# Optimization experiments

Measured on AMD Instinct MI355X. Metric: run time of the kernel, lower is better.

## Reference

```python
import jax, jax.numpy as jnp
import numpy as np

BS, EP = 32, 32
N_AGENTS, N_ATOM, EMBED = 8, 51, 32
STATE_DIM, HYP = 128, 64
V_MIN, V_MAX = -10.0, 10.0


def proj(support, probs, v_min, v_max, n_atom):
    # C51 categorical projection of (support, probs) onto the fixed atom grid
    # linspace(v_min, v_max, n_atom). support/probs: [..., M] -> [..., n_atom]
    support, probs = jnp.broadcast_arrays(support, probs)
    delta = (v_max - v_min) / (n_atom - 1)
    b = (jnp.clip(support, v_min, v_max) - v_min) / delta
    l = jnp.floor(b)
    u = jnp.ceil(b)
    eq = (u == l).astype(probs.dtype)  # support exactly on an atom -> all mass to l
    ml = probs * (u - b + eq)
    mu = probs * (b - l)
    shp = probs.shape
    n = int(np.prod(shp[:-1]))
    m = shp[-1]
    rows = jnp.arange(n)[:, None]
    out = jnp.zeros((n, n_atom), probs.dtype)
    out = out.at[rows, l.astype(jnp.int32).reshape(n, m)].add(ml.reshape(n, m))
    out = out.at[rows, u.astype(jnp.int32).reshape(n, m)].add(mu.reshape(n, m))
    return out.reshape(shp[:-1] + (n_atom,))


def bconv(p, q):
    # Full 1D convolution of per-row categorical pmfs (sum of two random vars).
    # p: [N, L], q: [N, M] -> [N, L+M-1], via grouped conv (one group per row).
    N, L = p.shape
    M = q.shape[-1]
    out = jax.lax.conv_general_dilated(
        p[None], jnp.flip(q, -1)[:, None, :],
        window_strides=(1,), padding=[(M - 1, M - 1)],
        feature_group_count=N, dimension_numbers=('NCW', 'OIW', 'NCW'))
    return out[0]


def mlp2(x, w1, b1, w2, b2):
    return jax.nn.relu(x @ w1.T + b1) @ w2.T + b2


def setup_inputs():
    key = jax.random.key(0)
    ks = jax.random.split(key, 20)
    def p(k, shape, s=0.05):
        return jax.random.normal(k, shape, dtype=jnp.float32) * s
    aq = jax.random.uniform(ks[0], (BS, EP, N_AGENTS, N_ATOM), dtype=jnp.float32)
    aq = aq / jnp.sum(aq, -1, keepdims=True)  # valid categorical distributions
    return {
        'agent_qs_distri': aq,
        'states': p(ks[1], (BS, EP, STATE_DIM), 1.0),
        'hw1_w1': p(ks[2], (HYP, STATE_DIM)), 'hw1_b1': p(ks[3], (HYP,)),
        'hw1_w2': p(ks[4], (EMBED * N_AGENTS, HYP)), 'hw1_b2': p(ks[5], (EMBED * N_AGENTS,)),
        'hb1_w': p(ks[6], (EMBED, STATE_DIM)), 'hb1_b': p(ks[7], (EMBED,)),
        'hwf_w1': p(ks[8], (HYP, STATE_DIM)), 'hwf_b1': p(ks[9], (HYP,)),
        'hwf_w2': p(ks[10], (EMBED, HYP)), 'hwf_b2': p(ks[11], (EMBED,)),
        'v_w1': p(ks[12], (EMBED, STATE_DIM)), 'v_b1': p(ks[13], (EMBED,)),
        'v_w2': p(ks[14], (1, EMBED)), 'v_b2': p(ks[15], (1,)),
    }


def reference(agent_qs_distri, states, hw1_w1, hw1_b1, hw1_w2, hw1_b2,
              hb1_w, hb1_b, hwf_w1, hwf_b1, hwf_w2, hwf_b2,
              v_w1, v_b1, v_w2, v_b2):
    bs, ep, n_agents, n_atom = agent_qs_distri.shape
    s = states.reshape(-1, STATE_DIM)
    atoms = jnp.linspace(V_MIN, V_MAX, n_atom).astype(jnp.float32)  # [A]

    w1 = jnp.abs(mlp2(s, hw1_w1, hw1_b1, hw1_w2, hw1_b2)).reshape(bs, ep, EMBED, n_agents)
    b1 = (s @ hb1_w.T + hb1_b).reshape(bs, ep, EMBED)

    # stage 1: scale each agent's support by w1[..., k, i], project back onto atoms
    sup1 = atoms * w1[..., None]                                       # [bs,ep,E,Na,A]
    aw = proj(sup1, agent_qs_distri[:, :, None], V_MIN, V_MAX, n_atom)  # [bs,ep,E,Na,A]
    awf = aw.reshape(-1, n_agents, n_atom)                              # [bs*ep*E,Na,A]
    q = awf[:, 0]
    for i in range(1, n_agents):
        q = bconv(q, awf[:, i])                                         # [.., Na*A-Na+1]
    L1 = n_agents * n_atom - n_agents + 1
    sup = jnp.linspace(n_agents * V_MIN, n_agents * V_MAX, L1).astype(jnp.float32)
    sup = jax.nn.elu(sup + b1[..., None])                               # [bs,ep,E,L1]
    x = proj(sup, q.reshape(bs, ep, EMBED, L1), V_MIN, V_MAX, n_atom)   # [bs,ep,E,A]

    # stage 2: hyper_w_final scaling, convolve across embed dim, add V(s)
    wf = jnp.abs(mlp2(s, hwf_w1, hwf_b1, hwf_w2, hwf_b2)).reshape(bs, ep, EMBED)
    xw = proj(atoms * wf[..., None], x, V_MIN, V_MAX, n_atom)           # [bs,ep,E,A]
    xwf = xw.reshape(-1, EMBED, n_atom)
    q = xwf[:, 0]
    for i in range(1, EMBED):
        q = bconv(q, xwf[:, i])                                         # [bs*ep, E*A-E+1]
    L2 = EMBED * n_atom - EMBED + 1
    v = mlp2(s, v_w1, v_b1, v_w2, v_b2).reshape(bs, ep, 1)
    sup2 = jnp.linspace(EMBED * V_MIN, EMBED * V_MAX, L2).astype(jnp.float32) + v
    return proj(sup2, q.reshape(bs, ep, L2), V_MIN, V_MAX, n_atom)      # [bs,ep,A]
```

## Files before the change

kernel.cpp:

```cpp
#include <hip/hip_runtime.h>
#include <hip/hip_bf16.h>
#include <math.h>

typedef unsigned short u16;

#define WAVE_SYNC() asm volatile("s_waitcnt lgkmcnt(0)" ::: "memory")

__device__ __forceinline__ float bf2f(u16 u) {
  union { unsigned int i; float f; } c;
  c.i = ((unsigned int)u) << 16;
  return c.f;
}
__device__ __forceinline__ float bflo(unsigned int u) {
  union { unsigned int i; float f; } c; c.i = u << 16; return c.f;
}
__device__ __forceinline__ float bfhi(unsigned int u) {
  union { unsigned int i; float f; } c; c.i = u & 0xffff0000u; return c.f;
}
__device__ __forceinline__ u16 f2bf(float f) {
  union { float f; unsigned int i; } c;
  c.f = f;
  unsigned int x = c.i;
  unsigned int r = (x + 0x7fffu + ((x >> 16) & 1u)) >> 16;
  return (u16)r;
}

__device__ __forceinline__ void proj_bounds(float wv, int& ML, int& MH) {
  float smin = (-10.0f + 0.4f * 0.0f)  * wv;
  float smax = (-10.0f + 0.4f * 50.0f) * wv;
  float bmin = (fminf(fmaxf(smin, -10.0f), 10.0f) + 10.0f) / 0.4f;
  float bmax = (fminf(fmaxf(smax, -10.0f), 10.0f) + 10.0f) / 0.4f;
  ML = (int)floorf(bmin);
  MH = (int)ceilf(bmax);
}

__device__ __forceinline__ void conv_pad2(const float* __restrict__ q,
                                          float* __restrict__ qn,
                                          const float* __restrict__ kvs,
                                          int ML, int W, int T,
                                          int LQ, int HQ, int Jmax,
                                          int tid, int nthr)
{
  const int Lout = LQ + ML;
  const int Hout = min(HQ + ML + T, Jmax);
  for (int J = Lout + tid; J <= Hout; J += nthr) {
    const float* qp = q + (J - ML);
    float acc = 0.f;
    for (int c = 0; c < W; c += 4) {
      float4 k4 = *(const float4*)(kvs + c);
      acc = fmaf(k4.x, qp[-c],     acc);
      acc = fmaf(k4.y, qp[-c - 1], acc);
      acc = fmaf(k4.z, qp[-c - 2], acc);
      acc = fmaf(k4.w, qp[-c - 3], acc);
    }
    qn[J] = acc;
  }
}

__device__ __forceinline__ void conv16(const float* __restrict__ q,
                                       float* __restrict__ qn,
                                       const float* __restrict__ kvs,
                                       int ML, int T,
                                       int LQ, int HQ, int Jmax,
                                       int tid, int nthr)
{
  const int Lout = LQ + ML;
  const int Hout = min(HQ + ML + T, Jmax);
  for (int J = Lout + tid; J <= Hout; J += nthr) {
    const float* qp = q + (J - ML);
    float a0 = 0.f, a1 = 0.f;
#pragma unroll
    for (int c = 0; c < 16; c += 4) {
      float4 k4 = *(const float4*)(kvs + c);
      a0 = fmaf(k4.x, qp[-c],     a0);
      a1 = fmaf(k4.y, qp[-c - 1], a1);
      a0 = fmaf(k4.z, qp[-c - 2], a0);
      a1 = fmaf(k4.w, qp[-c - 3], a1);
    }
    qn[J] = a0 + a1;
  }
}

__device__ __forceinline__ void conv8(const float* __restrict__ q,
                                      float* __restrict__ qn,
                                      const float* __restrict__ kvs,
                                      int ML, int T,
                                      int LQ, int HQ, int Jmax,
                                      int tid, int nthr)
{
  const int Lout = LQ + ML;
  const int Hout = min(HQ + ML + T, Jmax);
  for (int J = Lout + tid; J <= Hout; J += nthr) {
    const float* qp = q + (J - ML);
    float a0 = 0.f, a1 = 0.f;
#pragma unroll
    for (int c = 0; c < 8; c += 4) {
      float4 k4 = *(const float4*)(kvs + c);
      a0 = fmaf(k4.x, qp[-c],     a0);
      a1 = fmaf(k4.y, qp[-c - 1], a1);
      a0 = fmaf(k4.z, qp[-c - 2], a0);
      a1 = fmaf(k4.w, qp[-c - 3], a1);
    }
    qn[J] = a0 + a1;
  }
}

template<int TA, int TB>
__device__ __forceinline__ float gather_part(const float* __restrict__ pb,
                                             float wv, float j)
{
  float a0 = 0.f, a1 = 0.f, a2 = 0.f, a3 = 0.f;
  const float4* pb4 = (const float4*)pb;
  const float base = 25.0f - j;
#pragma unroll
  for (int t4 = TA; t4 < TB; ++t4) {
    float4 p4 = pb4[t4];
#define G1(PX, TT, AC) { \
    float sup = ((float)(TT) * 0.4f - 10.0f) * wv; \
    float c   = fminf(fmaxf(sup, -10.0f), 10.0f); \
    float d   = fmaf(c, 2.5f, base); \
    AC = fmaf(PX, fmaxf(0.f, 1.0f - fabsf(d)), AC); }
    G1(p4.x, 4 * t4 + 0, a0)
    G1(p4.y, 4 * t4 + 1, a1)
    G1(p4.z, 4 * t4 + 2, a2)
    G1(p4.w, 4 * t4 + 3, a3)
#undef G1
  }
  return (a0 + a1) + (a2 + a3);
}

template<int BF>
__device__ __forceinline__ float ldt(const void* p, int i) {
  if (BF) return bf2f(((const u16*)p)[i]);
  return ((const float*)p)[i];
}

template<int BF>
__device__ __forceinline__ float dot128_t(const void* w, int row, const float* s) {
  float acc = 0.f;
  if (BF) {
    const uint4* p = (const uint4*)((const u16*)w + row * 128);
#pragma unroll
    for (int i = 0; i < 16; ++i) {
      uint4 v = p[i];
      int b = i * 8;
      acc = fmaf(bflo(v.x), s[b + 0], acc); acc = fmaf(bfhi(v.x), s[b + 1], acc);
      acc = fmaf(bflo(v.y), s[b + 2], acc); acc = fmaf(bfhi(v.y), s[b + 3], acc);
      acc = fmaf(bflo(v.z), s[b + 4], acc); acc = fmaf(bfhi(v.z), s[b + 5], acc);
      acc = fmaf(bflo(v.w), s[b + 6], acc); acc = fmaf(bfhi(v.w), s[b + 7], acc);
    }
  } else {
    const float4* p = (const float4*)((const float*)w + row * 128);
#pragma unroll
    for (int i = 0; i < 32; ++i) {
      float4 v = p[i];
      int b = i * 4;
      acc = fmaf(v.x, s[b + 0], acc); acc = fmaf(v.y, s[b + 1], acc);
      acc = fmaf(v.z, s[b + 2], acc); acc = fmaf(v.w, s[b + 3], acc);
    }
  }
  return acc;
}

template<int BF>
__device__ __forceinline__ float dot64_t(const void* w, int row, const float* h) {
  float acc = 0.f;
  if (BF) {
    const uint4* p = (const uint4*)((const u16*)w + row * 64);
#pragma unroll
    for (int i = 0; i < 8; ++i) {
      uint4 v = p[i];
      int b = i * 8;
      acc = fmaf(bflo(v.x), h[b + 0], acc); acc = fmaf(bfhi(v.x), h[b + 1], acc);
      acc = fmaf(bflo(v.y), h[b + 2], acc); acc = fmaf(bfhi(v.y), h[b + 3], acc);
      acc = fmaf(bflo(v.z), h[b + 4], acc); acc = fmaf(bfhi(v.z), h[b + 5], acc);
      acc = fmaf(bflo(v.w), h[b + 6], acc); acc = fmaf(bfhi(v.w), h[b + 7], acc);
    }
  } else {
    const float4* p = (const float4*)((const float*)w + row * 64);
#pragma unroll
    for (int i = 0; i < 16; ++i) {
      float4 v = p[i];
      int b = i * 4;
      acc = fmaf(v.x, h[b + 0], acc); acc = fmaf(v.y, h[b + 1], acc);
      acc = fmaf(v.z, h[b + 2], acc); acc = fmaf(v.w, h[b + 3], acc);
    }
  }
  return acc;
}

template<int BF>
__device__ __forceinline__ void mlp_par(
    const void* states,
    const void* hw1_w1, const void* hw1_b1, const void* hw1_w2, const void* hw1_b2,
    const void* hb1_w,  const void* hb1_b,
    const void* hwf_w1, const void* hwf_b1, const void* hwf_w2, const void* hwf_b2,
    const void* v_w1,   const void* v_b1,   const void* v_w2,   const void* v_b2,
    float* w1_ws, float* b1_ws, float* wf_ws, float* v_ws,
    float* s_st, float* h1, float* hf, float* vh, int n, int tid)
{
  if (tid < 128) s_st[tid] = ldt<BF>(states, n * 128 + tid);
  __syncthreads();
  if (tid < 64)
    h1[tid] = fmaxf(dot128_t<BF>(hw1_w1, tid, s_st) + ldt<BF>(hw1_b1, tid), 0.f);
  else if (tid < 128)
    hf[tid - 64] = fmaxf(dot128_t<BF>(hwf_w1, tid - 64, s_st) + ldt<BF>(hwf_b1, tid - 64), 0.f);
  else if (tid < 160)
    vh[tid - 128] = fmaxf(dot128_t<BF>(v_w1, tid - 128, s_st) + ldt<BF>(v_b1, tid - 128), 0.f);
  else if (tid < 192)
    b1_ws[n * 32 + tid - 160] = dot128_t<BF>(hb1_w, tid - 160, s_st) + ldt<BF>(hb1_b, tid - 160);
  __syncthreads();
  if (tid < 256)
    w1_ws[n * 256 + tid] = fabsf(dot64_t<BF>(hw1_w2, tid, h1) + ldt<BF>(hw1_b2, tid));
  else if (tid < 288)
    wf_ws[n * 32 + tid - 256] = fabsf(dot64_t<BF>(hwf_w2, tid - 256, hf) + ldt<BF>(hwf_b2, tid - 256));
  else {
    int l2 = tid - 288;
    float part = vh[l2] * ldt<BF>(v_w2, l2);
    part += __shfl_xor(part, 1);  part += __shfl_xor(part, 2);
    part += __shfl_xor(part, 4);  part += __shfl_xor(part, 8);
    part += __shfl_xor(part, 16);
    if (l2 == 0) v_ws[n] = part + ldt<BF>(v_b2, 0);
  }
}

__global__ __launch_bounds__(320) void k_mlp(
    const void* __restrict__ states,
    const void* __restrict__ hw1_w1, const void* __restrict__ hw1_b1,
    const void* __restrict__ hw1_w2, const void* __restrict__ hw1_b2,
    const void* __restrict__ hb1_w,  const void* __restrict__ hb1_b,
    const void* __restrict__ hwf_w1, const void* __restrict__ hwf_b1,
    const void* __restrict__ hwf_w2, const void* __restrict__ hwf_b2,
    const void* __restrict__ v_w1,   const void* __restrict__ v_b1,
    const void* __restrict__ v_w2,   const void* __restrict__ v_b2,
    float* __restrict__ w1_ws, float* __restrict__ b1_ws,
    float* __restrict__ wf_ws, float* __restrict__ v_ws,
    int* __restrict__ flag)
{
  __shared__ float s_st[128];
  __shared__ float h1[64], hf[64], vh[32];
  __shared__ int sh_flag;
  const int n = blockIdx.x;
  const int tid = threadIdx.x;

  if (tid < 64) {
    const u16* sr = (const u16*)states;
    unsigned int e0 = (sr[tid] >> 7) & 0xFF;
    unsigned int e1 = (sr[tid + 64] >> 7) & 0xFF;
    unsigned long long bl0 = __ballot(e0 >= 97 && e0 <= 141);
    unsigned long long bl1 = __ballot(e1 >= 97 && e1 <= 141);
    int bfv = (__popcll(bl0) + __popcll(bl1) >= 104) ? 1 : 0;
    if (tid == 0) { sh_flag = bfv; *flag = bfv; }
  }
  __syncthreads();
  const int bf = sh_flag;

  if (bf)
    mlp_par<1>(states, hw1_w1, hw1_b1, hw1_w2, hw1_b2, hb1_w, hb1_b,
               hwf_w1, hwf_b1, hwf_w2, hwf_b2, v_w1, v_b1, v_w2, v_b2,
               w1_ws, b1_ws, wf_ws, v_ws, s_st, h1, hf, vh, n, tid);
  else
    mlp_par<0>(states, hw1_w1, hw1_b1, hw1_w2, hw1_b2, hb1_w, hb1_b,
               hwf_w1, hwf_b1, hwf_w2, hwf_b2, v_w1, v_b1, v_w2, v_b2,
               w1_ws, b1_ws, wf_ws, v_ws, s_st, h1, hf, vh, n, tid);
}

__global__ __launch_bounds__(128) void k_perembed(
    const void* __restrict__ aq,
    const float* __restrict__ w1_ws, const float* __restrict__ b1_ws,
    const float* __restrict__ wf_ws, float* __restrict__ xw_ws,
    const int* __restrict__ flag)
{
  __shared__ __align__(16) float P[8 * 52];
  __shared__ __align__(16) float TS[2][1344];

  const int tid  = threadIdx.x;
  const int w    = tid >> 6;
  const int lane = tid & 63;
  const int task = blockIdx.x * 2 + w;
  const int n = task >> 5;
  const int e = task & 31;
  const int bf = *flag;

  if (bf) {
    const u16* p = (const u16*)aq + n * 408;
    if (lane < 52) {
#pragma unroll
      for (int k = 0; k < 4; ++k) {
        int a = 4 * w + k;
        P[a * 52 + lane] = (lane < 51) ? bf2f(p[a * 51 + lane]) : 0.f;
      }
    }
  } else {
    const float* p = (const float*)aq + n * 408;
    if (lane < 52) {
#pragma unroll
      for (int k = 0; k < 4; ++k) {
        int a = 4 * w + k;
        P[a * 52 + lane] = (lane < 51) ? p[a * 51 + lane] : 0.f;
      }
    }
  }
  float wreg = (lane < 8) ? w1_ws[n * 256 + e * 8 + lane] : 0.f;
  float b1v  = b1_ws[n * 32 + e];
  float wfv  = wf_ws[n * 32 + e];

  int tgmax = (int)ceilf((90.0f - b1v) * 2.5f);
  if (tgmax < 0) tgmax = 0;
  const int Jcap = 64 + tgmax - 1;

  int mlA = 0, mhA = 0;
  if (lane < 8) proj_bounds(wreg, mlA, mhA);
  __syncthreads();

  float* Ab    = TS[w];
  float* Bb    = Ab + 520;
  float* kv    = Ab + 1040;
  float* kvo   = Ab + 1168;
  float* x2    = Ab + 1224;
  float* g     = Ab + 1276;
  float* kvsum = Ab + 1332;

#pragma unroll
  for (int r = 0; r < 2; ++r) {
    int a  = 4 * r + (lane >> 4);
    int jj = lane & 15;
    float wv = __shfl(wreg, a);
    int ML = __shfl(mlA, a);
    int MH = __shfl(mhA, a);
    int T  = MH - ML;
    float K = (25.0f - (float)(ML + jj)) - 25.0f * wv;
    float a0 = 0.f, a1 = 0.f, a2 = 0.f, a3 = 0.f;
    const float4* pb4 = (const float4*)(P + a * 52);
#pragma unroll
    for (int t4 = 0; t4 < 13; ++t4) {
      float4 p4 = pb4[t4];
      float d0 = fmaf((float)(4 * t4 + 0), wv, K);
      float d1 = fmaf((float)(4 * t4 + 1), wv, K);
      float d2 = fmaf((float)(4 * t4 + 2), wv, K);
      float d3 = fmaf((float)(4 * t4 + 3), wv, K);
      a0 = fmaf(p4.x, fmaxf(0.f, 1.0f - fabsf(d0)), a0);
      a1 = fmaf(p4.y, fmaxf(0.f, 1.0f - fabsf(d1)), a1);
      a2 = fmaf(p4.z, fmaxf(0.f, 1.0f - fabsf(d2)), a2);
      a3 = fmaf(p4.w, fmaxf(0.f, 1.0f - fabsf(d3)), a3);
    }
    float tot = (jj <= T) ? ((a0 + a1) + (a2 + a3)) : 0.f;
    if (T <= 15) {
      kv[a * 16 + jj] = tot;
      float s = tot;
      s += __shfl_xor(s, 1); s += __shfl_xor(s, 2);
      s += __shfl_xor(s, 4); s += __shfl_xor(s, 8);
      if (jj == 0) kvsum[a] = s;
    }
  }
  WAVE_SYNC();

  int LQ, HQ;
  float* q = Ab;
  float* qn = Bb;
  {
    float wv0 = __shfl(wreg, 0);
    int ML0 = __shfl(mlA, 0), MH0 = __shfl(mhA, 0);
    int T0 = MH0 - ML0;
    if (T0 <= 15) {
      if (lane <= T0 && 64 + ML0 + lane <= Jcap)
        Ab[64 + ML0 + lane] = kv[lane];
    } else {
      float acc = gather_part<0, 13>(P, wv0, (float)(ML0 + lane));
      float s = (lane <= T0) ? acc : 0.f;
#pragma unroll
      for (int d = 1; d < 64; d <<= 1) s += __shfl_xor(s, d);
      if (lane == 0) kvsum[0] = s;
      if (lane <= T0 && 64 + ML0 + lane <= Jcap)
        Ab[64 + ML0 + lane] = acc;
    }
    WAVE_SYNC();
    LQ = 64 + ML0; HQ = 64 + MH0;
  }

  for (int a = 1; a < 8; ++a) {
    float wv = __shfl(wreg, a);
    int ML = __shfl(mlA, a), MH = __shfl(mhA, a);
    int T = MH - ML;
    const float* kvs;
    int W;
    if (T <= 15) {
      kvs = kv + a * 16;
      W = (T <= 7) ? 8 : 16;
    } else {
      float acc = gather_part<0, 13>(P + a * 52, wv, (float)(ML + lane));
      float s = (lane <= T) ? acc : 0.f;
#pragma unroll
      for (int d = 1; d < 64; d <<= 1) s += __shfl_xor(s, d);
      if (lane == 0) kvsum[a] = s;
      W = (T + 4) & ~3;
      if (lane < W) kvo[lane] = (lane <= T) ? acc : 0.f;
      kvs = kvo;
    }
    if (lane < W - 1) q[LQ - 1 - lane] = 0.f;
    if (lane < T)     q[HQ + 1 + lane] = 0.f;
    WAVE_SYNC();
    if (T <= 7)       conv8 (q, qn, kvs, ML, T, LQ, HQ, Jcap, lane, 64);
    else if (T <= 15) conv16(q, qn, kvs, ML, T, LQ, HQ, Jcap, lane, 64);
    else              conv_pad2(q, qn, kvs, ML, W, T, LQ, HQ, Jcap, lane, 64);
    WAVE_SYNC();
    LQ += ML; HQ += MH;
    float* t_ = q; q = qn; qn = t_;
  }

  {
    if (lane < 53) g[lane] = 0.f;
    WAVE_SYNC();
    int top  = min(HQ, Jcap);
    int span = top - LQ + 1;
    float wsum = 0.f;
    for (int base = 0; base < span; base += 64) {
      int t = base + lane;
      if (t < span) {
        int tg = (LQ - 64) + t;
        float raw = (-80.0f + 0.4f * (float)tg) + b1v;
        float sup = (raw > 0.f) ? raw : expm1f(raw);
        float c  = fminf(fmaxf(sup, -10.0f), 10.0f);
        float b  = (c + 10.0f) / 0.4f;
        float l  = floorf(b);
        float u  = ceilf(b);
        float eq = (u == l) ? 1.0f : 0.0f;
        float p  = q[LQ + t];
        int   li = (int)l;
        wsum += p;
        atomicAdd(&g[li],     p * (u - b + eq));
        atomicAdd(&g[li + 1], p * (b - l));
      }
    }
#pragma unroll
    for (int d = 1; d < 64; d <<= 1) wsum += __shfl_xor(wsum, d);
    float tots = kvsum[0];
#pragma unroll
    for (int a2 = 1; a2 < 8; ++a2) tots *= kvsum[a2];
    WAVE_SYNC();
    if (lane == 0) g[50] += tots - wsum;
    WAVE_SYNC();
  }
  if (lane < 52) x2[lane] = (lane < 51) ? g[lane] : 0.f;
  WAVE_SYNC();

  {
    int MLf, MHf;
    proj_bounds(wfv, MLf, MHf);
    int Tf = MHf - MLf;
    if (Tf <= 15) {
      int q4 = lane >> 4, jj = lane & 15;
      float K = (25.0f - (float)(MLf + jj)) - 25.0f * wfv;
      float acc = 0.f;
#pragma unroll
      for (int k = 0; k < 13; ++k) {
        int t = q4 + 4 * k;
        float d = fmaf((float)t, wfv, K);
        acc = fmaf(x2[t], fmaxf(0.f, 1.0f - fabsf(d)), acc);
      }
      acc += __shfl_xor(acc, 16);
      acc += __shfl_xor(acc, 32);
      if (lane <= Tf)
        xw_ws[task * 51 + MLf + lane] = acc;
    } else {
      float acc = gather_part<0, 13>(x2, wfv, (float)(MLf + lane));
      if (lane <= Tf)
        xw_ws[task * 51 + MLf + lane] = acc;
    }
  }
}

__global__ __launch_bounds__(512) void k_final(
    const float* __restrict__ xw_ws, const float* __restrict__ wf_ws,
    const float* __restrict__ v_ws,
    void* __restrict__ out, const int* __restrict__ flag)
{
  __shared__ __align__(16) float bufA[4608];
  __shared__ __align__(16) float bufB[4608];
  __shared__ int meta_s[63];
  __shared__ int meta_l[63];
  __shared__ int meta_ml[32];
  __shared__ int meta_g[6];
  __shared__ int meta_mltot;
  __shared__ float gA[53];

  const int n    = blockIdx.x;
  const int tid  = threadIdx.x;
  const int lane = tid & 63;
  const int bf   = *flag;

  float vv = v_ws[n];

  for (int i = tid; i < 4608; i += 512) { bufA[i] = 0.f; bufB[i] = 0.f; }
  if (tid < 53) gA[tid] = 0.f;

  if (tid < 64) {
    float wfreg = (lane < 32) ? wf_ws[n * 32 + lane] : 0.f;
    int ml, mh;
    proj_bounds(wfreg, ml, mh);
    if (lane < 32) meta_ml[lane] = ml;
    int msum = ml;
#pragma unroll
    for (int d = 1; d < 32; d <<= 1) msum += __shfl_xor(msum, d);
    if (lane == 0) meta_mltot = msum;

    int curlen = mh - ml + 1;
    int base = 0, Ncur = 32;
#pragma unroll
    for (int c = 0; c <= 5; ++c) {
      int lm = (lane < Ncur) ? curlen : 0;
#pragma unroll
      for (int d = 1; d < 32; d <<= 1) {
        int o = __shfl_xor(lm, d);
        lm = (o > lm) ? o : lm;
      }
      int G = (lm + 11) & ~3;
      int sp = ((curlen + 3) & ~3) + G;
      int inc = (lane < Ncur) ? sp : 0;
      int v0 = inc;
#pragma unroll
      for (int d = 1; d < 32; d <<= 1) {
        int u = __shfl_up(inc, d);
        if (lane >= d && lane < 32) inc += u;
      }
      if (lane < Ncur) {
        meta_s[base + lane] = 832 + (inc - v0);
        meta_l[base + lane] = curlen;
      }
      if (lane == 0) meta_g[c] = G;
      if (c < 5) {
        int l0 = __shfl(curlen, 2 * lane);
        int l1 = __shfl(curlen, 2 * lane + 1);
        curlen = l0 + l1 - 1;
        base += Ncur;
        Ncur >>= 1;
      }
    }
  }
  __syncthreads();

  {
    int g = tid >> 4, i3 = tid & 15;
    int s2 = meta_s[g], l2 = meta_l[g], ml = meta_ml[g];
    const float* row = xw_ws + (n * 32 + g) * 51 + ml;
    for (int i0 = i3; i0 < l2; i0 += 16) bufA[s2 + i0] = row[i0];
  }
  __syncthreads();

#pragma unroll
  for (int c = 1; c <= 5; ++c) {
    const float* bin = (c & 1) ? bufA : bufB;
    float*       bout = (c & 1) ? bufB : bufA;
    const int Nout = 32 >> c;
    const int lg = 4 + c;
    const int gs = 1 << lg;
    const int k  = tid >> lg;
    const int st = tid & (gs - 1);
    const int bc = 64 - (64 >> c);
    const int bp = 64 - (64 >> (c - 1));
    const int i0 = bp + 2 * k;
    const int sA = meta_s[i0];
    const int sB = meta_s[i0 + 1];
    const int lB = meta_l[i0 + 1];
    const int sO = meta_s[bc + k];
    const int lO = meta_l[bc + k];
    const int W  = (lB + 3) & ~3;
    const int W4 = W >> 2;

    for (int j = st * 4; j < lO; j += gs * 4) {
      const float* Abase = bin + sA + j;
      float a0 = 0.f, a1 = 0.f, a2 = 0.f, a3 = 0.f;
      float q0 = Abase[3],  q1 = Abase[2],  q2 = Abase[1],  q3 = Abase[0],
            q4 = Abase[-1], q5 = Abase[-2], q6 = Abase[-3];
      const float4* kb = (const float4*)(bin + sB);
      for (int g = 0; g < W4; ++g) {
        float4 k4 = kb[g];
        a0 = fmaf(k4.x, q3, a0); a1 = fmaf(k4.x, q2, a1);
        a2 = fmaf(k4.x, q1, a2); a3 = fmaf(k4.x, q0, a3);
        a0 = fmaf(k4.y, q4, a0); a1 = fmaf(k4.y, q3, a1);
        a2 = fmaf(k4.y, q2, a2); a3 = fmaf(k4.y, q1, a3);
        a0 = fmaf(k4.z, q5, a0); a1 = fmaf(k4.z, q4, a1);
        a2 = fmaf(k4.z, q3, a2); a3 = fmaf(k4.z, q2, a3);
        a0 = fmaf(k4.w, q6, a0); a1 = fmaf(k4.w, q5, a1);
        a2 = fmaf(k4.w, q4, a2); a3 = fmaf(k4.w, q3, a3);
        q0 = q4; q1 = q5; q2 = q6;
        int b2 = -4 - 4 * g;
        q3 = Abase[b2];     q4 = Abase[b2 - 1];
        q5 = Abase[b2 - 2]; q6 = Abase[b2 - 3];
      }
      bout[sO + j] = a0;
      if (j + 1 < lO) bout[sO + j + 1] = a1;
      if (j + 2 < lO) bout[sO + j + 2] = a2;
      if (j + 3 < lO) bout[sO + j + 3] = a3;
    }

    if (c >= 2 && c <= 4) {
      int G = meta_g[c];
      for (int p = tid; p < G; p += 512) bout[832 - G + p] = 0.f;
      for (int k2 = 0; k2 < Nout; ++k2) {
        int ss = meta_s[bc + k2] + meta_l[bc + k2];
        int ee = (k2 + 1 < Nout) ? meta_s[bc + k2 + 1]
                                 : ss + G + 3;
        for (int p = ss + tid; p < ee; p += 512) bout[p] = 0.f;
      }
    }
    __syncthreads();
  }

  {
    int s5 = meta_s[62], l5 = meta_l[62], mlt = meta_mltot;
    const float* qf = bufB + s5;
    for (int t = tid; t < l5; t += 512) {
      int tg = mlt + t;
      float sup = (-320.0f + 0.4f * (float)tg) + vv;
      float c  = fminf(fmaxf(sup, -10.0f), 10.0f);
      float b  = (c + 10.0f) / 0.4f;
      float l  = floorf(b);
      float u  = ceilf(b);
      float eq = (u == l) ? 1.0f : 0.0f;
      float p  = qf[t];
      int   li = (int)l;
      atomicAdd(&gA[li],     p * (u - b + eq));
      atomicAdd(&gA[li + 1], p * (b - l));
    }
  }
  __syncthreads();
  if (tid < 51) {
    float o = gA[tid];
    if (bf) ((u16*)out)[n * 51 + tid] = f2bf(o);
    else    ((float*)out)[n * 51 + tid] = o;
  }
}

extern "C" void kernel_launch(void* const* d_in, const int* in_sizes, int n_in,
                              void* d_out, int out_size, void* d_ws, size_t ws_size,
                              hipStream_t stream)
{
  float* ws    = (float*)d_ws;
  float* w1_ws = ws;
  float* b1_ws = w1_ws + 1024 * 256;
  float* wf_ws = b1_ws + 1024 * 32;
  float* v_ws  = wf_ws + 1024 * 32;
  float* xw_ws = v_ws  + 1024;
  int*   flag  = (int*)(xw_ws + 1024 * 32 * 51);

  k_mlp<<<1024, 320, 0, stream>>>(d_in[1],
      d_in[2], d_in[3], d_in[4], d_in[5], d_in[6], d_in[7],
      d_in[8], d_in[9], d_in[10], d_in[11], d_in[12], d_in[13],
      d_in[14], d_in[15],
      w1_ws, b1_ws, wf_ws, v_ws, flag);

  k_perembed<<<16384, 128, 0, stream>>>(d_in[0], w1_ws, b1_ws, wf_ws, xw_ws, flag);

  k_final<<<1024, 512, 0, stream>>>(xw_ws, wf_ws, v_ws, d_out, flag);
}
```

Before: 250.3 us.

## Process two embed tasks per wavefront using half-wave lanes in perembed

Restructures the per-embed kernel so each 64-lane wavefront handles two (n,e) tasks, one per 32-lane half, doubling tasks per block and halving the grid. Loops and reductions are rewritten for 32-lane strides, and conv8 is dropped in favour of conv16 for small kernels. The goal is better lane utilisation, since many convolution spans are short and left most of a 64-wide wave idle. In exchange, long spans now take more iterations, LDS per block doubles, and a clamp on tgmax and HQ changes edge handling.

```diff
diff --git a/kernel.cpp b/kernel.cpp
--- a/kernel.cpp
+++ b/kernel.cpp
@@ -71,30 +71,6 @@
     float a0 = 0.f, a1 = 0.f;
 #pragma unroll
     for (int c = 0; c < 16; c += 4) {
-      float4 k4 = *(const float4*)(kvs + c);
-      a0 = fmaf(k4.x, qp[-c],     a0);
-      a1 = fmaf(k4.y, qp[-c - 1], a1);
-      a0 = fmaf(k4.z, qp[-c - 2], a0);
-      a1 = fmaf(k4.w, qp[-c - 3], a1);
-    }
-    qn[J] = a0 + a1;
-  }
-}
-
-__device__ __forceinline__ void conv8(const float* __restrict__ q,
-                                      float* __restrict__ qn,
-                                      const float* __restrict__ kvs,
-                                      int ML, int T,
-                                      int LQ, int HQ, int Jmax,
-                                      int tid, int nthr)
-{
-  const int Lout = LQ + ML;
-  const int Hout = min(HQ + ML + T, Jmax);
-  for (int J = Lout + tid; J <= Hout; J += nthr) {
-    const float* qp = q + (J - ML);
-    float a0 = 0.f, a1 = 0.f;
-#pragma unroll
-    for (int c = 0; c < 8; c += 4) {
       float4 k4 = *(const float4*)(kvs + c);
       a0 = fmaf(k4.x, qp[-c],     a0);
       a1 = fmaf(k4.y, qp[-c - 1], a1);
@@ -272,12 +248,15 @@
     const int* __restrict__ flag)
 {
   __shared__ __align__(16) float P[8 * 52];
-  __shared__ __align__(16) float TS[2][1344];
-
-  const int tid  = threadIdx.x;
-  const int w    = tid >> 6;
-  const int lane = tid & 63;
-  const int task = blockIdx.x * 2 + w;
+  __shared__ __align__(16) float TS[4][1344];
+
+  const int tid   = threadIdx.x;
+  const int wit   = tid >> 6;
+  const int lane  = tid & 63;
+  const int hl    = lane & 31;
+  const int hbase = lane & 32;
+  const int tno   = 2 * wit + (lane >> 5);
+  const int task  = blockIdx.x * 4 + tno;
   const int n = task >> 5;
   const int e = task & 31;
   const int bf = *flag;
@@ -287,7 +266,7 @@
     if (lane < 52) {
 #pragma unroll
       for (int k = 0; k < 4; ++k) {
-        int a = 4 * w + k;
+        int a = 4 * wit + k;
         P[a * 52 + lane] = (lane < 51) ? bf2f(p[a * 51 + lane]) : 0.f;
       }
     }
@@ -296,24 +275,24 @@
     if (lane < 52) {
 #pragma unroll
       for (int k = 0; k < 4; ++k) {
-        int a = 4 * w + k;
+        int a = 4 * wit + k;
         P[a * 52 + lane] = (lane < 51) ? p[a * 51 + lane] : 0.f;
       }
     }
   }
-  float wreg = (lane < 8) ? w1_ws[n * 256 + e * 8 + lane] : 0.f;
+  float wreg = (hl < 8) ? w1_ws[n * 256 + e * 8 + hl] : 0.f;
   float b1v  = b1_ws[n * 32 + e];
   float wfv  = wf_ws[n * 32 + e];
 
   int tgmax = (int)ceilf((90.0f - b1v) * 2.5f);
-  if (tgmax < 0) tgmax = 0;
+  tgmax = max(0, min(tgmax, 400));
   const int Jcap = 64 + tgmax - 1;
 
   int mlA = 0, mhA = 0;
-  if (lane < 8) proj_bounds(wreg, mlA, mhA);
+  if (hl < 8) proj_bounds(wreg, mlA, mhA);
   __syncthreads();
 
-  float* Ab    = TS[w];
+  float* Ab    = TS[tno];
   float* Bb    = Ab + 520;
   float* kv    = Ab + 1040;
   float* kvo   = Ab + 1168;
@@ -321,13 +300,12 @@
   float* g     = Ab + 1276;
   float* kvsum = Ab + 1332;
 
-#pragma unroll
-  for (int r = 0; r < 2; ++r) {
-    int a  = 4 * r + (lane >> 4);
-    int jj = lane & 15;
-    float wv = __shfl(wreg, a);
-    int ML = __shfl(mlA, a);
-    int MH = __shfl(mhA, a);
+  for (int r = 0; r < 4; ++r) {
+    int a  = 2 * r + ((hl >> 4) & 1);
+    int jj = hl & 15;
+    float wv = __shfl(wreg, hbase + a);
+    int ML = __shfl(mlA, hbase + a);
+    int MH = __shfl(mhA, hbase + a);
     int T  = MH - ML;
     float K = (25.0f - (float)(ML + jj)) - 25.0f * wv;
     float a0 = 0.f, a1 = 0.f, a2 = 0.f, a3 = 0.f;
@@ -359,63 +337,74 @@
   float* q = Ab;
   float* qn = Bb;
   {
-    float wv0 = __shfl(wreg, 0);
-    int ML0 = __shfl(mlA, 0), MH0 = __shfl(mhA, 0);
+    float wv0 = __shfl(wreg, hbase);
+    int ML0 = __shfl(mlA, hbase), MH0 = __shfl(mhA, hbase);
     int T0 = MH0 - ML0;
     if (T0 <= 15) {
-      if (lane <= T0 && 64 + ML0 + lane <= Jcap)
-        Ab[64 + ML0 + lane] = kv[lane];
+      if (hl <= T0 && 64 + ML0 + hl <= Jcap) Ab[64 + ML0 + hl] = kv[hl];
     } else {
-      float acc = gather_part<0, 13>(P, wv0, (float)(ML0 + lane));
-      float s = (lane <= T0) ? acc : 0.f;
-#pragma unroll
-      for (int d = 1; d < 64; d <<= 1) s += __shfl_xor(s, d);
-      if (lane == 0) kvsum[0] = s;
-      if (lane <= T0 && 64 + ML0 + lane <= Jcap)
-        Ab[64 + ML0 + lane] = acc;
+      float s = 0.f;
+      for (int b2 = 0; b2 <= T0; b2 += 32) {
+        int j = b2 + hl;
+        if (j <= T0) {
+          float acc = gather_part<0, 13>(P, wv0, (float)(ML0 + j));
+          s += acc;
+          if (64 + ML0 + j <= Jcap) Ab[64 + ML0 + j] = acc;
+        }
+      }
+      s += __shfl_xor(s, 1); s += __shfl_xor(s, 2); s += __shfl_xor(s, 4);
+      s += __shfl_xor(s, 8); s += __shfl_xor(s, 16);
+      if (hl == 0) kvsum[0] = s;
     }
     WAVE_SYNC();
     LQ = 64 + ML0; HQ = 64 + MH0;
   }
 
   for (int a = 1; a < 8; ++a) {
-    float wv = __shfl(wreg, a);
-    int ML = __shfl(mlA, a), MH = __shfl(mhA, a);
+    float wv = __shfl(wreg, hbase + a);
+    int ML = __shfl(mlA, hbase + a), MH = __shfl(mhA, hbase + a);
     int T = MH - ML;
     const float* kvs;
     int W;
     if (T <= 15) {
       kvs = kv + a * 16;
-      W = (T <= 7) ? 8 : 16;
+      W = 16;
     } else {
-      float acc = gather_part<0, 13>(P + a * 52, wv, (float)(ML + lane));
-      float s = (lane <= T) ? acc : 0.f;
-#pragma unroll
-      for (int d = 1; d < 64; d <<= 1) s += __shfl_xor(s, d);
-      if (lane == 0) kvsum[a] = s;
       W = (T + 4) & ~3;
-      if (lane < W) kvo[lane] = (lane <= T) ? acc : 0.f;
+      float s = 0.f;
+      for (int b2 = 0; b2 < W; b2 += 32) {
+        int j = b2 + hl;
+        float acc = 0.f;
+        if (j <= T) {
+          acc = gather_part<0, 13>(P + a * 52, wv, (float)(ML + j));
+          s += acc;
+        }
+        if (j < W) kvo[j] = acc;
+      }
+      s += __shfl_xor(s, 1); s += __shfl_xor(s, 2); s += __shfl_xor(s, 4);
+      s += __shfl_xor(s, 8); s += __shfl_xor(s, 16);
+      if (hl == 0) kvsum[a] = s;
       kvs = kvo;
     }
-    if (lane < W - 1) q[LQ - 1 - lane] = 0.f;
-    if (lane < T)     q[HQ + 1 + lane] = 0.f;
+    int HQc = min(HQ, Jcap);
+    for (int i = hl; i < W - 1; i += 32) q[LQ - 1 - i] = 0.f;
+    for (int i = hl; i < T;     i += 32) q[HQc + 1 + i] = 0.f;
     WAVE_SYNC();
-    if (T <= 7)       conv8 (q, qn, kvs, ML, T, LQ, HQ, Jcap, lane, 64);
-    else if (T <= 15) conv16(q, qn, kvs, ML, T, LQ, HQ, Jcap, lane, 64);
-    else              conv_pad2(q, qn, kvs, ML, W, T, LQ, HQ, Jcap, lane, 64);
+    if (T <= 15) conv16(q, qn, kvs, ML, T, LQ, HQc, Jcap, hl, 32);
+    else         conv_pad2(q, qn, kvs, ML, W, T, LQ, HQc, Jcap, hl, 32);
     WAVE_SYNC();
     LQ += ML; HQ += MH;
     float* t_ = q; q = qn; qn = t_;
   }
 
   {
-    if (lane < 53) g[lane] = 0.f;
+    for (int i = hl; i < 53; i += 32) g[i] = 0.f;
     WAVE_SYNC();
     int top  = min(HQ, Jcap);
     int span = top - LQ + 1;
     float wsum = 0.f;
-    for (int base = 0; base < span; base += 64) {
-      int t = base + lane;
+    for (int base = 0; base < span; base += 32) {
+      int t = base + hl;
       if (t < span) {
         int tg = (LQ - 64) + t;
         float raw = (-80.0f + 0.4f * (float)tg) + b1v;
@@ -432,16 +421,17 @@
         atomicAdd(&g[li + 1], p * (b - l));
       }
     }
-#pragma unroll
-    for (int d = 1; d < 64; d <<= 1) wsum += __shfl_xor(wsum, d);
+    wsum += __shfl_xor(wsum, 1); wsum += __shfl_xor(wsum, 2);
+    wsum += __shfl_xor(wsum, 4); wsum += __shfl_xor(wsum, 8);
+    wsum += __shfl_xor(wsum, 16);
     float tots = kvsum[0];
 #pragma unroll
     for (int a2 = 1; a2 < 8; ++a2) tots *= kvsum[a2];
     WAVE_SYNC();
-    if (lane == 0) g[50] += tots - wsum;
+    if (hl == 0) g[50] += tots - wsum;
     WAVE_SYNC();
   }
-  if (lane < 52) x2[lane] = (lane < 51) ? g[lane] : 0.f;
+  for (int i = hl; i < 52; i += 32) x2[i] = (i < 51) ? g[i] : 0.f;
   WAVE_SYNC();
 
   {
@@ -449,23 +439,26 @@
     proj_bounds(wfv, MLf, MHf);
     int Tf = MHf - MLf;
     if (Tf <= 15) {
-      int q4 = lane >> 4, jj = lane & 15;
+      int q2 = (hl >> 4) & 1, jj = hl & 15;
       float K = (25.0f - (float)(MLf + jj)) - 25.0f * wfv;
       float acc = 0.f;
 #pragma unroll
-      for (int k = 0; k < 13; ++k) {
-        int t = q4 + 4 * k;
+      for (int k = 0; k < 26; ++k) {
+        int t = q2 + 2 * k;
         float d = fmaf((float)t, wfv, K);
         acc = fmaf(x2[t], fmaxf(0.f, 1.0f - fabsf(d)), acc);
       }
       acc += __shfl_xor(acc, 16);
-      acc += __shfl_xor(acc, 32);
-      if (lane <= Tf)
-        xw_ws[task * 51 + MLf + lane] = acc;
+      if (q2 == 0 && jj <= Tf)
+        xw_ws[task * 51 + MLf + jj] = acc;
     } else {
-      float acc = gather_part<0, 13>(x2, wfv, (float)(MLf + lane));
-      if (lane <= Tf)
-        xw_ws[task * 51 + MLf + lane] = acc;
+      for (int b2 = 0; b2 <= Tf; b2 += 32) {
+        int j = b2 + hl;
+        if (j <= Tf) {
+          float acc = gather_part<0, 13>(x2, wfv, (float)(MLf + j));
+          xw_ws[task * 51 + MLf + j] = acc;
+        }
+      }
     }
   }
 }
@@ -650,7 +643,7 @@
       d_in[14], d_in[15],
       w1_ws, b1_ws, wf_ws, v_ws, flag);
 
-  k_perembed<<<16384, 128, 0, stream>>>(d_in[0], w1_ws, b1_ws, wf_ws, xw_ws, flag);
+  k_perembed<<<8192, 128, 0, stream>>>(d_in[0], w1_ws, b1_ws, wf_ws, xw_ws, flag);
 
   k_final<<<1024, 512, 0, stream>>>(xw_ws, wf_ws, v_ws, d_out, flag);
 }
```

Result: slower. 264.7 us (+5.7%).
